# Optimization experiments

Hardware: AMD Instinct MI355X
Metric: run time of the kernel (lower is better)

## Reference

```python
import jax, jax.numpy as jnp
import numpy as np

B, S, D_MODEL, H = 4, 4096, 1024, 16
HD = D_MODEL // H  # head_dim = 64


def setup_inputs() -> dict:
    key = jax.random.key(0)
    kq, kk, kv, kw, kb = jax.random.split(key, 5)
    Q = jax.random.normal(kq, (B, S, D_MODEL), dtype=jnp.float32)
    K = jax.random.normal(kk, (B, S, D_MODEL), dtype=jnp.float32)
    V = jax.random.normal(kv, (B, S, D_MODEL), dtype=jnp.float32)
    # out_proj: nn.Linear(d_model, d_model)
    lim = 1.0 / np.sqrt(D_MODEL)
    W_out = jax.random.uniform(kw, (D_MODEL, D_MODEL), jnp.float32, -lim, lim)
    b_out = jax.random.uniform(kb, (D_MODEL,), jnp.float32, -lim, lim)
    return {"Q": Q, "K": K, "V": V, "W_out": W_out, "b_out": b_out}


def reference(Q, K, V, W_out, b_out):
    b, s, d = Q.shape
    # split heads: [B, H, S, HD]
    Qh = Q.reshape(b, s, H, HD).transpose(0, 2, 1, 3)
    Kh = K.reshape(b, s, H, HD).transpose(0, 2, 1, 3)
    Vh = V.reshape(b, s, H, HD).transpose(0, 2, 1, 3)
    # linear attention reorder: KV = K^T V -> [B, H, HD, HD]
    KV = jnp.einsum('bhsd,bhse->bhde', Kh, Vh)
    # z = Q @ KV -> [B, H, S, HD]
    z = jnp.einsum('bhsd,bhde->bhse', Qh, KV)
    # merge heads -> [B, S, D]
    z = z.transpose(0, 2, 1, 3).reshape(b, s, d)
    # out_proj (torch Linear: x @ W^T + b, here W_out stored [out,in])
    return z @ W_out.T + b_out
```

## Files before the change

### kernel.cpp

```cpp
#include <hip/hip_runtime.h>
#include <hip/hip_bf16.h>

#define B_ 4
#define S_ 4096
#define DM 1024
#define H_ 16
#define HD 64
#define BH (B_*H_)
#define SPLIT 16
#define CHUNK (S_/SPLIT)

typedef __attribute__((ext_vector_type(8))) __bf16 bf16x8;
typedef __attribute__((ext_vector_type(4))) __bf16 bf16x4;
typedef __attribute__((ext_vector_type(4))) float f32x4;

#define MFMA16(a,b,c) __builtin_amdgcn_mfma_f32_16x16x32_bf16((a),(b),(c),0,0,0)

__device__ __forceinline__ void gload_lds16(const void* g, void* l) {
  __builtin_amdgcn_global_load_lds(
      (const __attribute__((address_space(1))) void*)g,
      (__attribute__((address_space(3))) void*)l, 16, 0, 0);
}

__global__ __launch_bounds__(256)
void k1_kv_partial(const float* __restrict__ Qg,
                   const float* __restrict__ Kg,
                   const float* __restrict__ Vg,
                   float* __restrict__ partial,
                   __bf16* __restrict__ Qb) {
  constexpr int LDP = 264;
  __shared__ __align__(16) __bf16 Kt[64 * LDP];
  __shared__ __align__(16) __bf16 Vt[64 * LDP];
  const int bid = blockIdx.x;
  const int split = bid >> 6;
  const int bh = bid & (BH - 1);
  const int b = bh >> 4, h = bh & 15;
  const int s0 = split * CHUNK;
  const int t = threadIdx.x;
  const size_t base = ((size_t)b * S_ + s0) * DM + h * HD;
  const float* Kbase = Kg + base;
  const float* Vbase = Vg + base;
  const float* Qbase = Qg + base;
  __bf16* Qbb = Qb + base;
  const int c = t & 15, sr = t >> 4;
  const int d0 = c * 4;
#pragma unroll
  for (int it = 0; it < 16; ++it) {
    const int s = it * 16 + sr;
    f32x4 kv = *reinterpret_cast<const f32x4*>(Kbase + (size_t)s * DM + d0);
    f32x4 vv = *reinterpret_cast<const f32x4*>(Vbase + (size_t)s * DM + d0);
    f32x4 qv = *reinterpret_cast<const f32x4*>(Qbase + (size_t)s * DM + d0);
    bf16x4 qo;
#pragma unroll
    for (int j = 0; j < 4; ++j) {
      Kt[(d0 + j) * LDP + s] = (__bf16)kv[j];
      Vt[(d0 + j) * LDP + s] = (__bf16)vv[j];
      qo[j] = (__bf16)qv[j];
    }
    *reinterpret_cast<bf16x4*>(Qbb + (size_t)s * DM + d0) = qo;
  }
  __syncthreads();
  const int w = t >> 6, l = t & 63, lr = l & 15, lg = l >> 4;
  f32x4 acc[4] = {};
#pragma unroll
  for (int ks = 0; ks < 8; ++ks) {
    bf16x8 a = *reinterpret_cast<const bf16x8*>(&Kt[(w * 16 + lr) * LDP + ks * 32 + lg * 8]);
#pragma unroll
    for (int n = 0; n < 4; ++n) {
      bf16x8 bb = *reinterpret_cast<const bf16x8*>(&Vt[(n * 16 + lr) * LDP + ks * 32 + lg * 8]);
      acc[n] = MFMA16(a, bb, acc[n]);
    }
  }
  float* dst = partial + ((size_t)(split * BH + bh) << 12);
#pragma unroll
  for (int n = 0; n < 4; ++n)
#pragma unroll
    for (int r = 0; r < 4; ++r) {
      const int d = w * 16 + lg * 4 + r;
      const int e = n * 16 + lr;
      dst[d * 64 + e] = acc[n][r];
    }
}

__global__ __launch_bounds__(256)
void k2_kv_reduce(const float* __restrict__ partial,
                  __bf16* __restrict__ kvt) {
  const int bid = blockIdx.x;
  const int bh = bid >> 2, q = bid & 3;
  const int t = threadIdx.x;
#pragma unroll
  for (int i = 0; i < 4; ++i) {
    const int idx = q * 1024 + i * 256 + t;
    float s = 0.f;
#pragma unroll
    for (int sp = 0; sp < SPLIT; ++sp)
      s += partial[((size_t)(sp * BH + bh) << 12) + idx];
    kvt[((size_t)bh << 12) + idx] = (__bf16)s;
  }
}

__global__ __launch_bounds__(256)
void k25_u(const float* __restrict__ Wg,
           const __bf16* __restrict__ kvt,
           __bf16* __restrict__ Ut) {
  const int bid = blockIdx.x;
  const int bh = bid >> 2, nblk = bid & 3;
  const int b = bh >> 4, h = bh & 15;
  const int t = threadIdx.x, w = t >> 6, l = t & 63, lr = l & 15, lg = l >> 4;
  const int n0w = nblk * 256 + w * 64;
  const __bf16* kvb = kvt + ((size_t)bh << 12);
  f32x4 acc[4][4] = {};
#pragma unroll
  for (int ks = 0; ks < 2; ++ks) {
    bf16x8 bfr[4];
#pragma unroll
    for (int nf = 0; nf < 4; ++nf)
      bfr[nf] = *reinterpret_cast<const bf16x8*>(kvb + (nf * 16 + lr) * 64 + ks * 32 + lg * 8);
#pragma unroll
    for (int mf = 0; mf < 4; ++mf) {
      const int n = n0w + mf * 16 + lr;
      const float* wp = Wg + (size_t)n * DM + h * 64 + ks * 32 + lg * 8;
      f32x4 w0 = *reinterpret_cast<const f32x4*>(wp);
      f32x4 w1 = *reinterpret_cast<const f32x4*>(wp + 4);
      bf16x8 af;
#pragma unroll
      for (int j = 0; j < 4; ++j) { af[j] = (__bf16)w0[j]; af[4 + j] = (__bf16)w1[j]; }
#pragma unroll
      for (int nf = 0; nf < 4; ++nf)
        acc[mf][nf] = MFMA16(af, bfr[nf], acc[mf][nf]);
    }
  }
  __bf16* ub = Ut + ((size_t)b << 20);
#pragma unroll
  for (int mf = 0; mf < 4; ++mf)
#pragma unroll
    for (int nf = 0; nf < 4; ++nf)
#pragma unroll
      for (int r = 0; r < 4; ++r) {
        const int n = n0w + mf * 16 + lg * 4 + r;
        ub[(size_t)n * DM + h * 64 + nf * 16 + lr] = (__bf16)acc[mf][nf][r];
      }
}

__global__ __launch_bounds__(256)
void k4_out_gemm(const __bf16* __restrict__ Qb,
                 const __bf16* __restrict__ Ut,
                 const float* __restrict__ biasg,
                 float* __restrict__ outg) {
  __shared__ __align__(16) __bf16 Alds[128 * 64];
  __shared__ __align__(16) __bf16 Blds[128 * 64];
  const int bid = blockIdx.x;
  const int b = bid >> 8, rem = bid & 255;
  const int nblk = rem >> 5, mblk = rem & 31;
  const int m0 = mblk * 128, n0 = nblk * 128;
  const int t = threadIdx.x, wid = t >> 6, l = t & 63, lr = l & 15, lg = l >> 4;
  const int wr = wid >> 1, wc = wid & 1;
  const __bf16* Ab = Qb + (size_t)b * S_ * DM;
  const __bf16* Bb = Ut + ((size_t)b << 20);
  f32x4 acc[4][4] = {};

  for (int kt = 0; kt < 16; ++kt) {
    const int k0 = kt * 64;
#pragma unroll
    for (int it = 0; it < 4; ++it) {
      const int idx = it * 256 + t;
      const int row = idx >> 3, c = idx & 7;
      const int gc = c ^ (row & 7);
      gload_lds16((const void*)(Ab + (size_t)(m0 + row) * DM + k0 + gc * 8),
                  (void*)((char*)Alds + (it * 256 + wid * 64) * 16));
      gload_lds16((const void*)(Bb + (size_t)(n0 + row) * DM + k0 + gc * 8),
                  (void*)((char*)Blds + (it * 256 + wid * 64) * 16));
    }
    __syncthreads();
#pragma unroll
    for (int ks = 0; ks < 2; ++ks) {
      bf16x8 af[4], bfr[4];
#pragma unroll
      for (int mt = 0; mt < 4; ++mt) {
        const int row = wr * 64 + mt * 16 + lr;
        const int ch = (ks * 4 + lg) ^ (row & 7);
        af[mt] = *reinterpret_cast<const bf16x8*>((const char*)Alds + row * 128 + ch * 16);
      }
#pragma unroll
      for (int nt = 0; nt < 4; ++nt) {
        const int row = wc * 64 + nt * 16 + lr;
        const int ch = (ks * 4 + lg) ^ (row & 7);
        bfr[nt] = *reinterpret_cast<const bf16x8*>((const char*)Blds + row * 128 + ch * 16);
      }
#pragma unroll
      for (int mt = 0; mt < 4; ++mt)
#pragma unroll
        for (int nt = 0; nt < 4; ++nt)
          acc[mt][nt] = MFMA16(af[mt], bfr[nt], acc[mt][nt]);
    }
    __syncthreads();
  }

#pragma unroll
  for (int nt = 0; nt < 4; ++nt) {
    const int colg = n0 + wc * 64 + nt * 16 + lr;
    const float bv = biasg[colg];
#pragma unroll
    for (int mt = 0; mt < 4; ++mt)
#pragma unroll
      for (int r = 0; r < 4; ++r) {
        const int rowg = m0 + wr * 64 + mt * 16 + lg * 4 + r;
        outg[((size_t)b * S_ + rowg) * DM + colg] = acc[mt][nt][r] + bv;
      }
  }
}

extern "C" void kernel_launch(void* const* d_in, const int* in_sizes, int n_in,
                              void* d_out, int out_size, void* d_ws, size_t ws_size,
                              hipStream_t stream) {
  const float* Q = (const float*)d_in[0];
  const float* K = (const float*)d_in[1];
  const float* V = (const float*)d_in[2];
  const float* W = (const float*)d_in[3];
  const float* bias = (const float*)d_in[4];
  float* out = (float*)d_out;

  char* ws = (char*)d_ws;
  float* partial = (float*)ws;
  __bf16* kvt = (__bf16*)(ws + (16u << 20));
  __bf16* Ut  = (__bf16*)(ws + (16u << 20) + (512u << 10));
  __bf16* Qb  = (__bf16*)(ws + (25u << 20));

  hipLaunchKernelGGL(k1_kv_partial, dim3(SPLIT * BH), dim3(256), 0, stream, Q, K, V, partial, Qb);
  hipLaunchKernelGGL(k2_kv_reduce, dim3(BH * 4), dim3(256), 0, stream, partial, kvt);
  hipLaunchKernelGGL(k25_u, dim3(BH * 4), dim3(256), 0, stream, W, kvt, Ut);
  hipLaunchKernelGGL(k4_out_gemm, dim3(1024), dim3(256), 0, stream, Qb, Ut, bias, out);
}
```

Measured before the change: 121.3 us.

## Compute K^T V in fp32 FMA with double-buffered async LDS loads; split Q conversion

Rewrites the K^T V partial kernel to stream K and V in fp32 through double-buffered LDS using global_load_lds, and to accumulate with scalar FMAs instead of bf16 MFMA after a transposing LDS store. The Q fp32-to-bf16 conversion moves into its own elementwise kernel. SPLIT is halved to 8, so each block loops over 64-row sub-chunks. The aim is to remove the strided transposed LDS writes and overlap loads with compute, at the cost of an extra launch, fewer blocks, and slower FMA math in place of MFMA.

```diff
diff --git a/kernel.cpp b/kernel.cpp
--- a/kernel.cpp
+++ b/kernel.cpp
@@ -7,8 +7,9 @@
 #define H_ 16
 #define HD 64
 #define BH (B_*H_)
-#define SPLIT 16
+#define SPLIT 8
 #define CHUNK (S_/SPLIT)
+#define SUB 64
 
 typedef __attribute__((ext_vector_type(8))) __bf16 bf16x8;
 typedef __attribute__((ext_vector_type(4))) __bf16 bf16x4;
@@ -23,63 +24,80 @@
 }
 
 __global__ __launch_bounds__(256)
-void k1_kv_partial(const float* __restrict__ Qg,
-                   const float* __restrict__ Kg,
-                   const float* __restrict__ Vg,
-                   float* __restrict__ partial,
-                   __bf16* __restrict__ Qb) {
-  constexpr int LDP = 264;
-  __shared__ __align__(16) __bf16 Kt[64 * LDP];
-  __shared__ __align__(16) __bf16 Vt[64 * LDP];
-  const int bid = blockIdx.x;
-  const int split = bid >> 6;
-  const int bh = bid & (BH - 1);
+void k0_convq(const float* __restrict__ Qg, __bf16* __restrict__ Qb) {
+  const size_t t = (size_t)blockIdx.x * 256 + threadIdx.x;
+#pragma unroll
+  for (int it = 0; it < 4; ++it) {
+    const size_t i = (size_t)it * 1048576 + t;
+    f32x4 w = *reinterpret_cast<const f32x4*>(Qg + i * 4);
+    bf16x4 o;
+#pragma unroll
+    for (int j = 0; j < 4; ++j) o[j] = (__bf16)w[j];
+    *reinterpret_cast<bf16x4*>(Qb + i * 4) = o;
+  }
+}
+
+__global__ __launch_bounds__(256)
+void k1_kv(const float* __restrict__ Kg, const float* __restrict__ Vg,
+           float* __restrict__ partial) {
+  __shared__ __align__(16) float Kb[2][SUB][64];
+  __shared__ __align__(16) float Vb[2][SUB][64];
+  const int bid = blockIdx.x;
+  const int split = bid >> 6, bh = bid & 63;
   const int b = bh >> 4, h = bh & 15;
+  const int t = threadIdx.x, wid = t >> 6;
   const int s0 = split * CHUNK;
-  const int t = threadIdx.x;
-  const size_t base = ((size_t)b * S_ + s0) * DM + h * HD;
-  const float* Kbase = Kg + base;
-  const float* Vbase = Vg + base;
-  const float* Qbase = Qg + base;
-  __bf16* Qbb = Qb + base;
-  const int c = t & 15, sr = t >> 4;
-  const int d0 = c * 4;
-#pragma unroll
-  for (int it = 0; it < 16; ++it) {
-    const int s = it * 16 + sr;
-    f32x4 kv = *reinterpret_cast<const f32x4*>(Kbase + (size_t)s * DM + d0);
-    f32x4 vv = *reinterpret_cast<const f32x4*>(Vbase + (size_t)s * DM + d0);
-    f32x4 qv = *reinterpret_cast<const f32x4*>(Qbase + (size_t)s * DM + d0);
-    bf16x4 qo;
-#pragma unroll
-    for (int j = 0; j < 4; ++j) {
-      Kt[(d0 + j) * LDP + s] = (__bf16)kv[j];
-      Vt[(d0 + j) * LDP + s] = (__bf16)vv[j];
-      qo[j] = (__bf16)qv[j];
-    }
-    *reinterpret_cast<bf16x4*>(Qbb + (size_t)s * DM + d0) = qo;
-  }
-  __syncthreads();
-  const int w = t >> 6, l = t & 63, lr = l & 15, lg = l >> 4;
-  f32x4 acc[4] = {};
-#pragma unroll
-  for (int ks = 0; ks < 8; ++ks) {
-    bf16x8 a = *reinterpret_cast<const bf16x8*>(&Kt[(w * 16 + lr) * LDP + ks * 32 + lg * 8]);
-#pragma unroll
-    for (int n = 0; n < 4; ++n) {
-      bf16x8 bb = *reinterpret_cast<const bf16x8*>(&Vt[(n * 16 + lr) * LDP + ks * 32 + lg * 8]);
-      acc[n] = MFMA16(a, bb, acc[n]);
-    }
-  }
+  const float* Ksrc = Kg + ((size_t)b * S_ + s0) * DM + h * HD;
+  const float* Vsrc = Vg + ((size_t)b * S_ + s0) * DM + h * HD;
+  const int d0 = (t >> 4) * 4, e0 = (t & 15) * 4;
+  float acc[4][4] = {};
+
+  auto stage = [&](int bi, int sc) {
+    const char* Kp = (const char*)(Ksrc + (size_t)sc * SUB * DM);
+    const char* Vp = (const char*)(Vsrc + (size_t)sc * SUB * DM);
+#pragma unroll
+    for (int it = 0; it < 4; ++it) {
+      const int idx = it * 256 + t;
+      const int row = idx >> 4, ch = idx & 15;
+      const int ldso = (it * 256 + wid * 64) * 16;
+      gload_lds16((const void*)(Kp + (size_t)row * (DM * 4) + ch * 16),
+                  (void*)((char*)&Kb[bi][0][0] + ldso));
+      gload_lds16((const void*)(Vp + (size_t)row * (DM * 4) + ch * 16),
+                  (void*)((char*)&Vb[bi][0][0] + ldso));
+    }
+  };
+
+  stage(0, 0);
+  asm volatile("s_waitcnt vmcnt(0)" ::: "memory");
+  __builtin_amdgcn_s_barrier();
+
+  for (int hc = 0; hc < CHUNK / SUB; ++hc) {
+    const int cur = hc & 1;
+    if (hc + 1 < CHUNK / SUB) stage(cur ^ 1, hc + 1);
+    const float* Ks = &Kb[cur][0][0];
+    const float* Vs = &Vb[cur][0][0];
+#pragma unroll 8
+    for (int s = 0; s < SUB; ++s) {
+      f32x4 kv = *reinterpret_cast<const f32x4*>(Ks + s * 64 + d0);
+      f32x4 vv = *reinterpret_cast<const f32x4*>(Vs + s * 64 + e0);
+#pragma unroll
+      for (int i = 0; i < 4; ++i)
+#pragma unroll
+        for (int j = 0; j < 4; ++j)
+          acc[i][j] = fmaf(kv[i], vv[j], acc[i][j]);
+    }
+    asm volatile("s_waitcnt vmcnt(0)" ::: "memory");
+    __builtin_amdgcn_s_barrier();
+  }
+
   float* dst = partial + ((size_t)(split * BH + bh) << 12);
 #pragma unroll
-  for (int n = 0; n < 4; ++n)
-#pragma unroll
-    for (int r = 0; r < 4; ++r) {
-      const int d = w * 16 + lg * 4 + r;
-      const int e = n * 16 + lr;
-      dst[d * 64 + e] = acc[n][r];
-    }
+  for (int i = 0; i < 4; ++i) {
+    f32x4 o;
+#pragma unroll
+    for (int j = 0; j < 4; ++j) o[j] = acc[i][j];
+    *reinterpret_cast<f32x4*>(dst + (d0 + i) * 64 + e0) = o;
+  }
 }
 
 __global__ __launch_bounds__(256)
@@ -222,11 +240,12 @@
 
   char* ws = (char*)d_ws;
   float* partial = (float*)ws;
-  __bf16* kvt = (__bf16*)(ws + (16u << 20));
-  __bf16* Ut  = (__bf16*)(ws + (16u << 20) + (512u << 10));
-  __bf16* Qb  = (__bf16*)(ws + (25u << 20));
-
-  hipLaunchKernelGGL(k1_kv_partial, dim3(SPLIT * BH), dim3(256), 0, stream, Q, K, V, partial, Qb);
+  __bf16* kvt = (__bf16*)(ws + (8u << 20));
+  __bf16* Ut  = (__bf16*)(ws + (9u << 20));
+  __bf16* Qb  = (__bf16*)(ws + (17u << 20));
+
+  hipLaunchKernelGGL(k1_kv, dim3(SPLIT * BH), dim3(256), 0, stream, K, V, partial);
+  hipLaunchKernelGGL(k0_convq, dim3(4096), dim3(256), 0, stream, Q, Qb);
   hipLaunchKernelGGL(k2_kv_reduce, dim3(BH * 4), dim3(256), 0, stream, partial, kvt);
   hipLaunchKernelGGL(k25_u, dim3(BH * 4), dim3(256), 0, stream, W, kvt, Ut);
   hipLaunchKernelGGL(k4_out_gemm, dim3(1024), dim3(256), 0, stream, Qb, Ut, bias, out);
```

Measured after the change: 124.6 us. 1.03x slower.
